# Kernel optimization log

Measured on AMD Instinct MI355X. Metric: run time of the kernel, lower is better.

Reference implementation:

```python
import jax, jax.numpy as jnp
import numpy as np

N = 100000
E = 1600000
D_IN = 128
D_OUT = 128


def setup_inputs() -> dict:
    key = jax.random.key(0)
    k1, k2, k3, k4, k5, k6 = jax.random.split(key, 6)
    h = jax.random.normal(k1, (N, D_IN), dtype=jnp.float32)
    # deg^{-1/2}-style positive per-node normalization, shape [N,1]
    norm = jax.random.uniform(k2, (N, 1), dtype=jnp.float32, minval=0.05, maxval=1.0)
    weight = jax.random.normal(k3, (D_IN, D_OUT), dtype=jnp.float32) * (1.0 / np.sqrt(D_IN))
    bias = jax.random.normal(k4, (D_OUT,), dtype=jnp.float32) * 0.01
    src = jax.random.randint(k5, (E,), 0, N, dtype=jnp.int32)
    dst = jax.random.randint(k6, (E,), 0, N, dtype=jnp.int32)
    return {"h": h, "norm": norm, "weight": weight, "bias": bias, "src": src, "dst": dst}


def reference(h, norm, weight, bias, src, dst):
    # m = (h @ W) * norm   (per-source-node message)
    m = jnp.matmul(h, weight) * norm            # [N, D_OUT]
    # copy_src + sum: scatter-sum messages from src nodes into dst nodes
    n = jax.ops.segment_sum(m[src], dst, num_segments=h.shape[0])  # [N, D_OUT]
    # destination-side normalization, bias, LeakyReLU(0.2)
    n = n * norm + bias
    return jax.nn.leaky_relu(n, negative_slope=0.2)
```

## Files before the change

kernel.cpp:

```cpp
#include <hip/hip_runtime.h>

#define N_NODES 100000
#define E_EDGES 1600000
#define D 128
#define SHIFT 7
#define BNODES 128
#define NB ((N_NODES + BNODES - 1) / BNODES)

#define CNT_CHUNK 2048
#define CNT_NBLK ((E_EDGES + CNT_CHUNK - 1) / CNT_CHUNK)
#define PREP_NBLK (N_NODES * 32 / 256)
#define PREP1K (N_NODES * 32 / 1024)
#define SCAT_CHUNK 8192
#define SCAT_PASS 2
#define SCAT_NBLK ((E_EDGES + SCAT_CHUNK - 1) / SCAT_CHUNK)
#define GATHD_NBLK ((N_NODES + 63) / 64)
#define GATH32_NBLK (N_NODES / 8)

#define CAPB 2560

#define CAP_N 64
#define LSTR 65

#define GROWS 64
#define KCH 32

typedef _Float16       f16x8  __attribute__((ext_vector_type(8)));
typedef float          f32x4  __attribute__((ext_vector_type(4)));
typedef unsigned short u16x8  __attribute__((ext_vector_type(8)));

#define WS_CNT   0
#define WS_POS   784
#define WS_BOFF  1568
#define WS_NOFF  2356
#define WS_EBUF  102400
#define WS_WHS   (WS_EBUF + NB * CAPB)
#define WS_ESRC  (102400 + E_EDGES)
#define WS_HS    (102400 + 2 * E_EDGES)
#define WS_FULL_INTS ((size_t)WS_HS + (size_t)N_NODES * D / 2)
#define WS_MID_INTS  ((size_t)WS_HS)

#define GROW16 256

__global__ __launch_bounds__(1024) void prep_scatter(
    const float* __restrict__ h, const float* __restrict__ norm,
    unsigned short* __restrict__ hs, const int* __restrict__ src,
    const int* __restrict__ dst, int* __restrict__ bcnt,
    int* __restrict__ ebuf, int prep_blocks)
{
    __shared__ int hist[NB];
    const int t = threadIdx.x;
    if ((int)blockIdx.x < prep_blocks) {
        const int idx = blockIdx.x * 1024 + t;
        const int node = idx >> 5;
        const int c = (idx & 31) << 2;
        const float nv = norm[node];
        const float4 v = *reinterpret_cast<const float4*>(h + node * D + c);
        float a[4] = {v.x * nv, v.y * nv, v.z * nv, v.w * nv};
        ushort4 o;
        unsigned short* op = reinterpret_cast<unsigned short*>(&o);
        #pragma unroll
        for (int i = 0; i < 4; ++i) {
            unsigned int u = __float_as_uint(a[i]);
            u += 0x7FFFu + ((u >> 16) & 1u);
            op[i] = (unsigned short)(u >> 16);
        }
        *reinterpret_cast<ushort4*>(hs + node * D + c) = o;
        return;
    }
    const int cb = blockIdx.x - prep_blocks;
    const int e0 = cb * SCAT_CHUNK;
    const int rem = (E_EDGES - e0 < SCAT_CHUNK) ? (E_EDGES - e0) : SCAT_CHUNK;
    for (int i = t; i < NB; i += 1024) hist[i] = 0;
    __syncthreads();

    if (rem == SCAT_CHUNK) {
        const int4* d4 = reinterpret_cast<const int4*>(dst + e0);
        #pragma unroll
        for (int p = 0; p < SCAT_PASS; ++p) {
            const int4 vv = d4[p * 1024 + t];
            atomicAdd(&hist[vv.x >> SHIFT], 1);
            atomicAdd(&hist[vv.y >> SHIFT], 1);
            atomicAdd(&hist[vv.z >> SHIFT], 1);
            atomicAdd(&hist[vv.w >> SHIFT], 1);
        }
    } else {
        for (int i = t; i < rem; i += 1024)
            atomicAdd(&hist[dst[e0 + i] >> SHIFT], 1);
    }
    __syncthreads();

    if (t < NB) {
        const int c = hist[t];
        hist[t] = c ? atomicAdd(&bcnt[t], c) : 0;
    }
    __syncthreads();

    if (rem == SCAT_CHUNK) {
        const int4* d4 = reinterpret_cast<const int4*>(dst + e0);
        const int4* s4 = reinterpret_cast<const int4*>(src + e0);
        #pragma unroll
        for (int p = 0; p < SCAT_PASS; ++p) {
            const int4 dv = d4[p * 1024 + t];
            const int4 sv = s4[p * 1024 + t];
            int b, pz;
            b = dv.x >> SHIFT; pz = atomicAdd(&hist[b], 1);
            if (pz < CAPB) ebuf[b * CAPB + pz] = (sv.x << SHIFT) | (dv.x & (BNODES - 1));
            b = dv.y >> SHIFT; pz = atomicAdd(&hist[b], 1);
            if (pz < CAPB) ebuf[b * CAPB + pz] = (sv.y << SHIFT) | (dv.y & (BNODES - 1));
            b = dv.z >> SHIFT; pz = atomicAdd(&hist[b], 1);
            if (pz < CAPB) ebuf[b * CAPB + pz] = (sv.z << SHIFT) | (dv.z & (BNODES - 1));
            b = dv.w >> SHIFT; pz = atomicAdd(&hist[b], 1);
            if (pz < CAPB) ebuf[b * CAPB + pz] = (sv.w << SHIFT) | (dv.w & (BNODES - 1));
        }
    } else {
        for (int i = t; i < rem; i += 1024) {
            const int d = dst[e0 + i];
            const int b = d >> SHIFT;
            const int pz = atomicAdd(&hist[b], 1);
            if (pz < CAPB) ebuf[b * CAPB + pz] = (src[e0 + i] << SHIFT) | (d & (BNODES - 1));
        }
    }
}

__device__ __forceinline__ void wprep_body(int tid, const float* __restrict__ Wm,
                                           f16x8* __restrict__ Whs) {
    const int kiter = tid >> 9;
    const int nt = (tid >> 6) & 7;
    const int lane = tid & 63;
    const int q = lane >> 4;
    const int col = nt * 16 + (lane & 15);
    f16x8 v;
    #pragma unroll
    for (int j = 0; j < 8; ++j)
        v[j] = (_Float16)Wm[(kiter * 32 + q * 8 + j) * D + col];
    Whs[tid] = v;
}

__global__ __launch_bounds__(256) void gather_direct(
    const unsigned short* __restrict__ hs, const int* __restrict__ bcnt,
    const int* __restrict__ ebuf, _Float16* __restrict__ g16,
    const float* __restrict__ Wm, f16x8* __restrict__ Whs)
{
    if ((int)blockIdx.x >= GATHD_NBLK) {
        wprep_body((blockIdx.x - GATHD_NBLK) * 256 + threadIdx.x, Wm, Whs);
        return;
    }
    __shared__ int lists[64][LSTR];
    __shared__ int lcnt[64];
    const int t = threadIdx.x;
    const int g = blockIdx.x;
    const int bin = g >> 1;
    const int sub = g & 1;
    if (t < 64) lcnt[t] = 0;
    __syncthreads();
    int cnt = bcnt[bin];
    cnt = (cnt < 0) ? 0 : ((cnt > CAPB) ? CAPB : cnt);
    const int b0 = bin * CAPB;
    const int b1 = b0 + cnt;
    for (int i = b0 + t; i < b1; i += 256) {
        const int w = ebuf[i];
        const int l = w & (BNODES - 1);
        const unsigned s = (unsigned)w >> SHIFT;
        if ((l >> 6) == sub && s < (unsigned)N_NODES) {
            const int p = atomicAdd(&lcnt[l & 63], 1);
            if (p < CAP_N) lists[l & 63][p] = (int)s;
        }
    }
    __syncthreads();

    const int grp = t >> 4;
    const int c = (t & 15) << 3;

    #pragma unroll 1
    for (int r = 0; r < 4; ++r) {
        const int local = r * 16 + grp;
        const int node = g * 64 + local;
        const int deg = lcnt[local];
        float a[8];
        #pragma unroll
        for (int j = 0; j < 8; ++j) a[j] = 0.f;

        if (deg <= CAP_N) {
            const int* lp = lists[local];
            int i = 0;
            for (; i + 7 < deg; i += 8) {
                const int s0 = lp[i];     const int s1 = lp[i + 1];
                const int s2 = lp[i + 2]; const int s3 = lp[i + 3];
                const int s4 = lp[i + 4]; const int s5 = lp[i + 5];
                const int s6 = lp[i + 6]; const int s7 = lp[i + 7];
                const u16x8 u0 = *reinterpret_cast<const u16x8*>(hs + s0 * D + c);
                const u16x8 u1 = *reinterpret_cast<const u16x8*>(hs + s1 * D + c);
                const u16x8 u2 = *reinterpret_cast<const u16x8*>(hs + s2 * D + c);
                const u16x8 u3 = *reinterpret_cast<const u16x8*>(hs + s3 * D + c);
                const u16x8 u4 = *reinterpret_cast<const u16x8*>(hs + s4 * D + c);
                const u16x8 u5 = *reinterpret_cast<const u16x8*>(hs + s5 * D + c);
                const u16x8 u6 = *reinterpret_cast<const u16x8*>(hs + s6 * D + c);
                const u16x8 u7 = *reinterpret_cast<const u16x8*>(hs + s7 * D + c);
                #pragma unroll
                for (int j = 0; j < 8; ++j) {
                    a[j] += __uint_as_float((unsigned int)u0[j] << 16);
                    a[j] += __uint_as_float((unsigned int)u1[j] << 16);
                    a[j] += __uint_as_float((unsigned int)u2[j] << 16);
                    a[j] += __uint_as_float((unsigned int)u3[j] << 16);
                    a[j] += __uint_as_float((unsigned int)u4[j] << 16);
                    a[j] += __uint_as_float((unsigned int)u5[j] << 16);
                    a[j] += __uint_as_float((unsigned int)u6[j] << 16);
                    a[j] += __uint_as_float((unsigned int)u7[j] << 16);
                }
            }
            if (i + 3 < deg) {
                const int s0 = lp[i];     const int s1 = lp[i + 1];
                const int s2 = lp[i + 2]; const int s3 = lp[i + 3];
                const u16x8 u0 = *reinterpret_cast<const u16x8*>(hs + s0 * D + c);
                const u16x8 u1 = *reinterpret_cast<const u16x8*>(hs + s1 * D + c);
                const u16x8 u2 = *reinterpret_cast<const u16x8*>(hs + s2 * D + c);
                const u16x8 u3 = *reinterpret_cast<const u16x8*>(hs + s3 * D + c);
                #pragma unroll
                for (int j = 0; j < 8; ++j) {
                    a[j] += __uint_as_float((unsigned int)u0[j] << 16);
                    a[j] += __uint_as_float((unsigned int)u1[j] << 16);
                    a[j] += __uint_as_float((unsigned int)u2[j] << 16);
                    a[j] += __uint_as_float((unsigned int)u3[j] << 16);
                }
                i += 4;
            }
            for (; i < deg; ++i) {
                const int s = lp[i];
                const u16x8 u = *reinterpret_cast<const u16x8*>(hs + s * D + c);
                #pragma unroll
                for (int j = 0; j < 8; ++j)
                    a[j] += __uint_as_float((unsigned int)u[j] << 16);
            }
        } else {
            const int myl = (sub << 6) | local;
            for (int i = b0; i < b1; ++i) {
                const int w = ebuf[i];
                const unsigned s = (unsigned)w >> SHIFT;
                if ((w & (BNODES - 1)) == myl && s < (unsigned)N_NODES) {
                    const u16x8 u = *reinterpret_cast<const u16x8*>(hs + s * D + c);
                    #pragma unroll
                    for (int j = 0; j < 8; ++j)
                        a[j] += __uint_as_float((unsigned int)u[j] << 16);
                }
            }
        }

        if (node < N_NODES) {
            f16x8 o;
            #pragma unroll
            for (int j = 0; j < 8; ++j) o[j] = (_Float16)a[j];
            *reinterpret_cast<f16x8*>(g16 + node * GROW16 + c) = o;
        }
    }
}

__global__ __launch_bounds__(256) void gemm_mfma_f16g(
    const _Float16* g16, float* out, const f16x8* __restrict__ Whs,
    const float* __restrict__ bias, const float* __restrict__ norm)
{
    __shared__ f16x8 Wlds[2048];
    const int t = threadIdx.x;
    const int row0 = blockIdx.x * 64;

    #pragma unroll
    for (int p = 0; p < 8; ++p)
        reinterpret_cast<float4*>(Wlds)[p * 256 + t] =
            reinterpret_cast<const float4*>(Whs)[p * 256 + t];
    __syncthreads();

    const int lane = t & 63;
    const int strip = t >> 6;
    const int q = lane >> 4;
    const int l15 = lane & 15;

    int mrow = row0 + strip * 16 + l15;
    if (mrow >= N_NODES) mrow = N_NODES - 1;

    f32x4 acc[8];
    #pragma unroll
    for (int i = 0; i < 8; ++i) acc[i] = (f32x4){0.f, 0.f, 0.f, 0.f};

    #pragma unroll
    for (int kiter = 0; kiter < 4; ++kiter) {
        const f16x8 a =
            *reinterpret_cast<const f16x8*>(g16 + mrow * GROW16 + kiter * 32 + q * 8);
        #pragma unroll
        for (int nt = 0; nt < 8; ++nt) {
            const f16x8 b = Wlds[(kiter * 8 + nt) * 64 + lane];
            acc[nt] = __builtin_amdgcn_mfma_f32_16x16x32_f16(a, b, acc[nt], 0, 0, 0);
        }
    }

    __syncthreads();

    float nrm[4];
    int mr[4];
    #pragma unroll
    for (int rgi = 0; rgi < 4; ++rgi) {
        mr[rgi] = row0 + strip * 16 + q * 4 + rgi;
        nrm[rgi] = (mr[rgi] < N_NODES) ? norm[mr[rgi]] : 0.f;
    }
    #pragma unroll
    for (int nt = 0; nt < 8; ++nt) {
        const int col = nt * 16 + l15;
        const float bc = bias[col];
        #pragma unroll
        for (int rgi = 0; rgi < 4; ++rgi) {
            if (mr[rgi] < N_NODES) {
                float v = acc[nt][rgi] * nrm[rgi] + bc;
                v = v > 0.f ? v : 0.2f * v;
                out[mr[rgi] * D + col] = v;
            }
        }
    }
}

__global__ __launch_bounds__(256) void prep_count(const float* __restrict__ h,
                                                  const float* __restrict__ norm,
                                                  unsigned short* __restrict__ hs,
                                                  const int* __restrict__ dst,
                                                  int* __restrict__ cnt,
                                                  int prep_blocks) {
    __shared__ int hist[NB];
    const int t = threadIdx.x;
    if ((int)blockIdx.x < prep_blocks) {
        const int idx = blockIdx.x * 256 + t;
        const int node = idx >> 5;
        const int c = (idx & 31) << 2;
        const float nv = norm[node];
        const float4 v = *reinterpret_cast<const float4*>(h + node * D + c);
        float a[4] = {v.x * nv, v.y * nv, v.z * nv, v.w * nv};
        ushort4 o;
        unsigned short* op = reinterpret_cast<unsigned short*>(&o);
        #pragma unroll
        for (int i = 0; i < 4; ++i) {
            unsigned int u = __float_as_uint(a[i]);
            u += 0x7FFFu + ((u >> 16) & 1u);
            op[i] = (unsigned short)(u >> 16);
        }
        *reinterpret_cast<ushort4*>(hs + node * D + c) = o;
        return;
    }
    const int cb = blockIdx.x - prep_blocks;
    const int e0 = cb * CNT_CHUNK;
    const int rem = (E_EDGES - e0 < CNT_CHUNK) ? (E_EDGES - e0) : CNT_CHUNK;
    for (int i = t; i < NB; i += 256) hist[i] = 0;
    __syncthreads();
    if (rem == CNT_CHUNK) {
        const int4* d4 = reinterpret_cast<const int4*>(dst + e0);
        #pragma unroll
        for (int p = 0; p < 2; ++p) {
            const int4 v = d4[p * 256 + t];
            atomicAdd(&hist[v.x >> SHIFT], 1);
            atomicAdd(&hist[v.y >> SHIFT], 1);
            atomicAdd(&hist[v.z >> SHIFT], 1);
            atomicAdd(&hist[v.w >> SHIFT], 1);
        }
    } else {
        for (int i = t; i < rem; i += 256)
            atomicAdd(&hist[dst[e0 + i] >> SHIFT], 1);
    }
    __syncthreads();
    for (int b = t; b < NB; b += 256) {
        const int c = hist[b];
        if (c) atomicAdd(&cnt[b], c);
    }
}

__global__ __launch_bounds__(1024) void coarse_scan(const int* __restrict__ cnt,
                                                    int* __restrict__ boff,
                                                    int* __restrict__ pos) {
    __shared__ int buf[2][1024];
    const int t = threadIdx.x;
    const int v = (t < NB) ? cnt[t] : 0;
    int pi = 0;
    buf[0][t] = v;
    __syncthreads();
    #pragma unroll
    for (int o = 1; o < 1024; o <<= 1) {
        const int nv = buf[pi][t] + (t >= o ? buf[pi][t - o] : 0);
        buf[1 - pi][t] = nv;
        pi = 1 - pi;
        __syncthreads();
    }
    if (t < NB) {
        const int excl = buf[pi][t] - v;
        boff[t] = excl;
        pos[t] = excl;
    }
    if (t == 0) boff[NB] = E_EDGES;
}

__global__ __launch_bounds__(1024) void coarse_scatter(const int* __restrict__ src,
                                                       const int* __restrict__ dst,
                                                       int* __restrict__ pos,
                                                       int* __restrict__ ebuf) {
    __shared__ int hist[NB];
    const int t = threadIdx.x;
    const int e0 = blockIdx.x * SCAT_CHUNK;
    const int rem = (E_EDGES - e0 < SCAT_CHUNK) ? (E_EDGES - e0) : SCAT_CHUNK;
    for (int i = t; i < NB; i += 1024) hist[i] = 0;
    __syncthreads();
    if (rem == SCAT_CHUNK) {
        const int4* d4 = reinterpret_cast<const int4*>(dst + e0);
        #pragma unroll
        for (int p = 0; p < SCAT_PASS; ++p) {
            const int4 v = d4[p * 1024 + t];
            atomicAdd(&hist[v.x >> SHIFT], 1);
            atomicAdd(&hist[v.y >> SHIFT], 1);
            atomicAdd(&hist[v.z >> SHIFT], 1);
            atomicAdd(&hist[v.w >> SHIFT], 1);
        }
    } else {
        for (int i = t; i < rem; i += 1024)
            atomicAdd(&hist[dst[e0 + i] >> SHIFT], 1);
    }
    __syncthreads();
    for (int b = t; b < NB; b += 1024) {
        const int c = hist[b];
        if (c) hist[b] = atomicAdd(&pos[b], c);
    }
    __syncthreads();
    if (rem == SCAT_CHUNK) {
        const int4* d4 = reinterpret_cast<const int4*>(dst + e0);
        const int4* s4 = reinterpret_cast<const int4*>(src + e0);
        #pragma unroll
        for (int p = 0; p < SCAT_PASS; ++p) {
            const int4 dv = d4[p * 1024 + t];
            const int4 sv = s4[p * 1024 + t];
            int pz;
            pz = atomicAdd(&hist[dv.x >> SHIFT], 1);
            ebuf[pz] = (sv.x << SHIFT) | (dv.x & (BNODES - 1));
            pz = atomicAdd(&hist[dv.y >> SHIFT], 1);
            ebuf[pz] = (sv.y << SHIFT) | (dv.y & (BNODES - 1));
            pz = atomicAdd(&hist[dv.z >> SHIFT], 1);
            ebuf[pz] = (sv.z << SHIFT) | (dv.z & (BNODES - 1));
            pz = atomicAdd(&hist[dv.w >> SHIFT], 1);
            ebuf[pz] = (sv.w << SHIFT) | (dv.w & (BNODES - 1));
        }
    } else {
        for (int i = t; i < rem; i += 1024) {
            const int d = dst[e0 + i];
            const int b = d >> SHIFT;
            const int p = atomicAdd(&hist[b], 1);
            ebuf[p] = (src[e0 + i] << SHIFT) | (d & (BNODES - 1));
        }
    }
}

__global__ __launch_bounds__(256) void bin_sort(const int* __restrict__ boff,
                                                const int* __restrict__ ebuf,
                                                int* __restrict__ esrc,
                                                int* __restrict__ noff) {
    __shared__ int hist[BNODES];
    __shared__ int curs[BNODES];
    __shared__ int sbuf[2][BNODES];
    const int t = threadIdx.x;
    const int bin = blockIdx.x;
    if (t < BNODES) hist[t] = 0;
    __syncthreads();
    const int b0 = boff[bin];
    const int b1 = boff[bin + 1];
    for (int i = b0 + t; i < b1; i += 256)
        atomicAdd(&hist[ebuf[i] & (BNODES - 1)], 1);
    __syncthreads();
    if (t < BNODES) sbuf[0][t] = hist[t];
    __syncthreads();
    int pi = 0;
    #pragma unroll
    for (int o = 1; o < BNODES; o <<= 1) {
        if (t < BNODES)
            sbuf[1 - pi][t] = sbuf[pi][t] + (t >= o ? sbuf[pi][t - o] : 0);
        pi = 1 - pi;
        __syncthreads();
    }
    if (t < BNODES) {
        const int base = b0 + sbuf[pi][t] - hist[t];
        curs[t] = base;
        const int node = (bin << SHIFT) + t;
        if (node < N_NODES) noff[node] = base;
    }
    if (bin == 0 && t == 0) noff[N_NODES] = E_EDGES;
    __syncthreads();
    for (int i = b0 + t; i < b1; i += 256) {
        const int w = ebuf[i];
        const int p = atomicAdd(&curs[w & (BNODES - 1)], 1);
        esrc[p] = w >> SHIFT;
    }
}

__global__ __launch_bounds__(256) void gather_fp32(const float* __restrict__ h,
                                                   const float* __restrict__ norm,
                                                   const int* __restrict__ noff,
                                                   const int* __restrict__ esrc,
                                                   float* __restrict__ g,
                                                   const float* __restrict__ Wm,
                                                   f16x8* __restrict__ Whs) {
    if ((int)blockIdx.x >= GATH32_NBLK) {
        wprep_body((blockIdx.x - GATH32_NBLK) * 256 + threadIdx.x, Wm, Whs);
        return;
    }
    const int t = threadIdx.x;
    const int node = blockIdx.x * 8 + (t >> 5);
    const int c = (t & 31) << 2;
    const int beg = noff[node];
    const int end = noff[node + 1];
    float4 acc = make_float4(0.f, 0.f, 0.f, 0.f);
    for (int i = beg; i < end; ++i) {
        const int s = esrc[i];
        const float nv = norm[s];
        const float4 hv = *reinterpret_cast<const float4*>(h + s * D + c);
        acc.x += hv.x * nv;
        acc.y += hv.y * nv;
        acc.z += hv.z * nv;
        acc.w += hv.w * nv;
    }
    *reinterpret_cast<float4*>(g + node * D + c) = acc;
}

__global__ __launch_bounds__(256) void scatter_kernel(
    const float* __restrict__ h, const float* __restrict__ norm,
    const int* __restrict__ src, const int* __restrict__ dst,
    float* __restrict__ g)
{
    const int idx = blockIdx.x * 256 + threadIdx.x;
    const int e = idx >> 5;
    const int c = (idx & 31) << 2;
    const int s = src[e];
    const int d = dst[e];
    const float nv = norm[s];
    const float4 hv = *reinterpret_cast<const float4*>(h + s * D + c);
    float* gp = g + d * D + c;
    atomicAdd(gp + 0, hv.x * nv);
    atomicAdd(gp + 1, hv.y * nv);
    atomicAdd(gp + 2, hv.z * nv);
    atomicAdd(gp + 3, hv.w * nv);
}

__global__ __launch_bounds__(256) void gemm_mfma(
    float* __restrict__ out, const f16x8* __restrict__ Whs,
    const float* __restrict__ bias, const float* __restrict__ norm)
{
    __shared__ f16x8 Wlds[2048];
    const int t = threadIdx.x;
    const int row0 = blockIdx.x * 64;

    #pragma unroll
    for (int p = 0; p < 8; ++p)
        reinterpret_cast<float4*>(Wlds)[p * 256 + t] =
            reinterpret_cast<const float4*>(Whs)[p * 256 + t];
    __syncthreads();

    const int lane = t & 63;
    const int strip = t >> 6;
    const int q = lane >> 4;
    const int l15 = lane & 15;

    int mrow = row0 + strip * 16 + l15;
    if (mrow >= N_NODES) mrow = N_NODES - 1;

    f32x4 acc[8];
    #pragma unroll
    for (int i = 0; i < 8; ++i) acc[i] = (f32x4){0.f, 0.f, 0.f, 0.f};

    #pragma unroll
    for (int kiter = 0; kiter < 4; ++kiter) {
        const float* gp = out + mrow * D + kiter * 32 + q * 8;
        const float4 ga = *reinterpret_cast<const float4*>(gp);
        const float4 gb = *reinterpret_cast<const float4*>(gp + 4);
        f16x8 a;
        a[0] = (_Float16)ga.x; a[1] = (_Float16)ga.y;
        a[2] = (_Float16)ga.z; a[3] = (_Float16)ga.w;
        a[4] = (_Float16)gb.x; a[5] = (_Float16)gb.y;
        a[6] = (_Float16)gb.z; a[7] = (_Float16)gb.w;
        #pragma unroll
        for (int nt = 0; nt < 8; ++nt) {
            const f16x8 b = Wlds[(kiter * 8 + nt) * 64 + lane];
            acc[nt] = __builtin_amdgcn_mfma_f32_16x16x32_f16(a, b, acc[nt], 0, 0, 0);
        }
    }

    float nrm[4];
    int mr[4];
    #pragma unroll
    for (int rgi = 0; rgi < 4; ++rgi) {
        mr[rgi] = row0 + strip * 16 + q * 4 + rgi;
        nrm[rgi] = (mr[rgi] < N_NODES) ? norm[mr[rgi]] : 0.f;
    }
    #pragma unroll
    for (int nt = 0; nt < 8; ++nt) {
        const int col = nt * 16 + l15;
        const float bc = bias[col];
        #pragma unroll
        for (int rgi = 0; rgi < 4; ++rgi) {
            if (mr[rgi] < N_NODES) {
                float v = acc[nt][rgi] * nrm[rgi] + bc;
                v = v > 0.f ? v : 0.2f * v;
                out[mr[rgi] * D + col] = v;
            }
        }
    }
}

__global__ __launch_bounds__(256) void gemm_epilogue(
    float* __restrict__ out, const float* __restrict__ Wm,
    const float* __restrict__ bias, const float* __restrict__ norm)
{
    __shared__ float gs[GROWS][D + 4];
    __shared__ float Wlds[KCH][D];
    const int t = threadIdx.x;
    const int row0 = blockIdx.x * GROWS;

    #pragma unroll
    for (int p = 0; p < 8; ++p) {
        const int i = p * 256 + t;
        const int r = i >> 5;
        const int c = (i & 31) << 2;
        int gr = row0 + r;
        if (gr >= N_NODES) gr = N_NODES - 1;
        const float4 v = *reinterpret_cast<const float4*>(out + gr * D + c);
        *reinterpret_cast<float4*>(&gs[r][c]) = v;
    }

    const int rg = (t >> 5) * 8;
    const int cb = (t & 31) << 2;

    float4 acc[8];
    #pragma unroll
    for (int i = 0; i < 8; ++i) acc[i] = make_float4(0.f, 0.f, 0.f, 0.f);

    for (int kc = 0; kc < D; kc += KCH) {
        __syncthreads();
        #pragma unroll
        for (int p = 0; p < 4; ++p) {
            const int i = p * 256 + t;
            const int kk = i >> 5;
            const int c = (i & 31) << 2;
            *reinterpret_cast<float4*>(&Wlds[kk][c]) =
                *reinterpret_cast<const float4*>(Wm + (kc + kk) * D + c);
        }
        __syncthreads();

        #pragma unroll
        for (int k4 = 0; k4 < KCH; k4 += 4) {
            float4 wv[4];
            #pragma unroll
            for (int kk = 0; kk < 4; ++kk)
                wv[kk] = *reinterpret_cast<const float4*>(&Wlds[k4 + kk][cb]);
            #pragma unroll
            for (int i = 0; i < 8; ++i) {
                const float4 gv = *reinterpret_cast<const float4*>(&gs[rg + i][kc + k4]);
                acc[i].x += gv.x * wv[0].x; acc[i].y += gv.x * wv[0].y;
                acc[i].z += gv.x * wv[0].z; acc[i].w += gv.x * wv[0].w;
                acc[i].x += gv.y * wv[1].x; acc[i].y += gv.y * wv[1].y;
                acc[i].z += gv.y * wv[1].z; acc[i].w += gv.y * wv[1].w;
                acc[i].x += gv.z * wv[2].x; acc[i].y += gv.z * wv[2].y;
                acc[i].z += gv.z * wv[2].z; acc[i].w += gv.z * wv[2].w;
                acc[i].x += gv.w * wv[3].x; acc[i].y += gv.w * wv[3].y;
                acc[i].z += gv.w * wv[3].z; acc[i].w += gv.w * wv[3].w;
            }
        }
    }

    const float4 b = *reinterpret_cast<const float4*>(bias + cb);
    #pragma unroll
    for (int i = 0; i < 8; ++i) {
        const int gr = row0 + rg + i;
        if (gr < N_NODES) {
            const float nv = norm[gr];
            float4 v;
            v.x = acc[i].x * nv + b.x;
            v.y = acc[i].y * nv + b.y;
            v.z = acc[i].z * nv + b.z;
            v.w = acc[i].w * nv + b.w;
            v.x = v.x > 0.f ? v.x : 0.2f * v.x;
            v.y = v.y > 0.f ? v.y : 0.2f * v.y;
            v.z = v.z > 0.f ? v.z : 0.2f * v.z;
            v.w = v.w > 0.f ? v.w : 0.2f * v.w;
            *reinterpret_cast<float4*>(out + gr * D + cb) = v;
        }
    }
}

extern "C" void kernel_launch(void* const* d_in, const int* in_sizes, int n_in,
                              void* d_out, int out_size, void* d_ws, size_t ws_size,
                              hipStream_t stream) {
    const float* h    = (const float*)d_in[0];
    const float* norm = (const float*)d_in[1];
    const float* Wm   = (const float*)d_in[2];
    const float* bias = (const float*)d_in[3];
    const int*   src  = (const int*)d_in[4];
    const int*   dst  = (const int*)d_in[5];
    float* out = (float*)d_out;
    int* ws = (int*)d_ws;

    if (ws_size >= WS_MID_INTS * 4) {
        const bool use_bf16 = (ws_size >= WS_FULL_INTS * 4);

        if (use_bf16) {
            int* bcnt = ws + WS_CNT;
            int* ebuf = ws + WS_EBUF;
            f16x8* Whs = (f16x8*)(ws + WS_WHS);
            unsigned short* hs = (unsigned short*)(ws + WS_HS);
            _Float16* g16 = (_Float16*)out;

            hipMemsetAsync(bcnt, 0, 784 * sizeof(int), stream);
            prep_scatter<<<PREP1K + SCAT_NBLK, 1024, 0, stream>>>(
                h, norm, hs, src, dst, bcnt, ebuf, PREP1K);
            gather_direct<<<GATHD_NBLK + 8, 256, 0, stream>>>(hs, bcnt, ebuf, g16, Wm, Whs);
            gemm_mfma_f16g<<<(N_NODES + 63) / 64, 256, 0, stream>>>(g16, out, Whs, bias, norm);
        } else {
            int* cnt  = ws + WS_CNT;
            int* pos  = ws + WS_POS;
            int* boff = ws + WS_BOFF;
            int* noff = ws + WS_NOFF;
            int* ebuf = ws + WS_EBUF;
            int* esrc = ws + WS_ESRC;
            f16x8* Whs = (f16x8*)ebuf;
            hipMemsetAsync(cnt, 0, 784 * sizeof(int), stream);
            prep_count<<<CNT_NBLK, 256, 0, stream>>>(h, norm, (unsigned short*)ws, dst, cnt, 0);
            coarse_scan   <<<1, 1024, 0, stream>>>(cnt, boff, pos);
            coarse_scatter<<<SCAT_NBLK, 1024, 0, stream>>>(src, dst, pos, ebuf);
            bin_sort      <<<NB, 256, 0, stream>>>(boff, ebuf, esrc, noff);
            gather_fp32<<<GATH32_NBLK + 8, 256, 0, stream>>>(h, norm, noff, esrc, out, Wm, Whs);
            gemm_mfma<<<(N_NODES + 63) / 64, 256, 0, stream>>>(out, Whs, bias, norm);
        }
    } else {
        hipMemsetAsync(out, 0, (size_t)N_NODES * D * sizeof(float), stream);
        scatter_kernel<<<(E_EDGES * 32) / 256, 256, 0, stream>>>(h, norm, src, dst, out);
        gemm_epilogue<<<(N_NODES + GROWS - 1) / GROWS, 256, 0, stream>>>(out, Wm, bias, norm);
    }
}
```

Baseline: 218.7 us.

## Fuse neighbor gather with MFMA GEMM epilogue in one kernel via LDS staging

Merges the gather kernel and the GEMM kernel. Each block writes its aggregated fp16 rows into shared memory, reusing the edge-list buffer with its stride widened, then runs the MFMA matmul directly from LDS. This removes the fp16 intermediate round trip through global memory and one kernel launch. In exchange, every block converts the weight matrix from fp32 to fp16 itself in two halves, and the added LDS use may lower occupancy.

```diff
diff --git a/kernel.cpp b/kernel.cpp
--- a/kernel.cpp
+++ b/kernel.cpp
@@ -20,7 +20,7 @@
 #define CAPB 2560
 
 #define CAP_N 64
-#define LSTR 65
+#define LSTR 68
 
 #define GROWS 64
 #define KCH 32
@@ -34,13 +34,10 @@
 #define WS_BOFF  1568
 #define WS_NOFF  2356
 #define WS_EBUF  102400
-#define WS_WHS   (WS_EBUF + NB * CAPB)
 #define WS_ESRC  (102400 + E_EDGES)
 #define WS_HS    (102400 + 2 * E_EDGES)
 #define WS_FULL_INTS ((size_t)WS_HS + (size_t)N_NODES * D / 2)
 #define WS_MID_INTS  ((size_t)WS_HS)
-
-#define GROW16 256
 
 __global__ __launch_bounds__(1024) void prep_scatter(
     const float* __restrict__ h, const float* __restrict__ norm,
@@ -123,31 +120,17 @@
     }
 }
 
-__device__ __forceinline__ void wprep_body(int tid, const float* __restrict__ Wm,
-                                           f16x8* __restrict__ Whs) {
-    const int kiter = tid >> 9;
-    const int nt = (tid >> 6) & 7;
-    const int lane = tid & 63;
-    const int q = lane >> 4;
-    const int col = nt * 16 + (lane & 15);
-    f16x8 v;
-    #pragma unroll
-    for (int j = 0; j < 8; ++j)
-        v[j] = (_Float16)Wm[(kiter * 32 + q * 8 + j) * D + col];
-    Whs[tid] = v;
-}
-
-__global__ __launch_bounds__(256) void gather_direct(
+__global__ __launch_bounds__(256) void gather_gemm(
     const unsigned short* __restrict__ hs, const int* __restrict__ bcnt,
-    const int* __restrict__ ebuf, _Float16* __restrict__ g16,
-    const float* __restrict__ Wm, f16x8* __restrict__ Whs)
+    const int* __restrict__ ebuf, const float* __restrict__ Wm,
+    const float* __restrict__ bias, const float* __restrict__ norm,
+    float* __restrict__ out)
 {
-    if ((int)blockIdx.x >= GATHD_NBLK) {
-        wprep_body((blockIdx.x - GATHD_NBLK) * 256 + threadIdx.x, Wm, Whs);
-        return;
-    }
     __shared__ int lists[64][LSTR];
     __shared__ int lcnt[64];
+    __shared__ f16x8 Wlds[1024];
+    _Float16 (*gs)[136] = reinterpret_cast<_Float16 (*)[136]>(&lists[0][0]);
+
     const int t = threadIdx.x;
     const int g = blockIdx.x;
     const int bin = g >> 1;
@@ -175,7 +158,6 @@
     #pragma unroll 1
     for (int r = 0; r < 4; ++r) {
         const int local = r * 16 + grp;
-        const int node = g * 64 + local;
         const int deg = lcnt[local];
         float a[8];
         #pragma unroll
@@ -246,53 +228,51 @@
             }
         }
 
-        if (node < N_NODES) {
-            f16x8 o;
-            #pragma unroll
-            for (int j = 0; j < 8; ++j) o[j] = (_Float16)a[j];
-            *reinterpret_cast<f16x8*>(g16 + node * GROW16 + c) = o;
-        }
-    }
-}
-
-__global__ __launch_bounds__(256) void gemm_mfma_f16g(
-    const _Float16* g16, float* out, const f16x8* __restrict__ Whs,
-    const float* __restrict__ bias, const float* __restrict__ norm)
-{
-    __shared__ f16x8 Wlds[2048];
-    const int t = threadIdx.x;
-    const int row0 = blockIdx.x * 64;
-
-    #pragma unroll
-    for (int p = 0; p < 8; ++p)
-        reinterpret_cast<float4*>(Wlds)[p * 256 + t] =
-            reinterpret_cast<const float4*>(Whs)[p * 256 + t];
-    __syncthreads();
+        f16x8 o;
+        #pragma unroll
+        for (int j = 0; j < 8; ++j) o[j] = (_Float16)a[j];
+        *reinterpret_cast<f16x8*>(&gs[local][c]) = o;
+    }
 
     const int lane = t & 63;
     const int strip = t >> 6;
     const int q = lane >> 4;
     const int l15 = lane & 15;
-
-    int mrow = row0 + strip * 16 + l15;
-    if (mrow >= N_NODES) mrow = N_NODES - 1;
+    const int row0 = g * 64;
 
     f32x4 acc[8];
     #pragma unroll
     for (int i = 0; i < 8; ++i) acc[i] = (f32x4){0.f, 0.f, 0.f, 0.f};
 
-    #pragma unroll
-    for (int kiter = 0; kiter < 4; ++kiter) {
-        const f16x8 a =
-            *reinterpret_cast<const f16x8*>(g16 + mrow * GROW16 + kiter * 32 + q * 8);
-        #pragma unroll
-        for (int nt = 0; nt < 8; ++nt) {
-            const f16x8 b = Wlds[(kiter * 8 + nt) * 64 + lane];
-            acc[nt] = __builtin_amdgcn_mfma_f32_16x16x32_f16(a, b, acc[nt], 0, 0, 0);
-        }
-    }
-
-    __syncthreads();
+    #pragma unroll 1
+    for (int half = 0; half < 2; ++half) {
+        __syncthreads();
+        for (int e = t; e < 1024; e += 256) {
+            const int ge = (half << 10) + e;
+            const int kiter = ge >> 9;
+            const int nt = (ge >> 6) & 7;
+            const int lane2 = ge & 63;
+            const int q2 = lane2 >> 4;
+            const int col = nt * 16 + (lane2 & 15);
+            f16x8 v;
+            #pragma unroll
+            for (int j = 0; j < 8; ++j)
+                v[j] = (_Float16)Wm[(kiter * 32 + q2 * 8 + j) * D + col];
+            Wlds[e] = v;
+        }
+        __syncthreads();
+        #pragma unroll
+        for (int kk = 0; kk < 2; ++kk) {
+            const int kiter = half * 2 + kk;
+            const f16x8 a =
+                *reinterpret_cast<const f16x8*>(&gs[strip * 16 + l15][kiter * 32 + q * 8]);
+            #pragma unroll
+            for (int nt = 0; nt < 8; ++nt) {
+                const f16x8 b = Wlds[(kk * 8 + nt) * 64 + lane];
+                acc[nt] = __builtin_amdgcn_mfma_f32_16x16x32_f16(a, b, acc[nt], 0, 0, 0);
+            }
+        }
+    }
 
     float nrm[4];
     int mr[4];
@@ -488,6 +468,20 @@
         const int p = atomicAdd(&curs[w & (BNODES - 1)], 1);
         esrc[p] = w >> SHIFT;
     }
+}
+
+__device__ __forceinline__ void wprep_body(int tid, const float* __restrict__ Wm,
+                                           f16x8* __restrict__ Whs) {
+    const int kiter = tid >> 9;
+    const int nt = (tid >> 6) & 7;
+    const int lane = tid & 63;
+    const int q = lane >> 4;
+    const int col = nt * 16 + (lane & 15);
+    f16x8 v;
+    #pragma unroll
+    for (int j = 0; j < 8; ++j)
+        v[j] = (_Float16)Wm[(kiter * 32 + q * 8 + j) * D + col];
+    Whs[tid] = v;
 }
 
 __global__ __launch_bounds__(256) void gather_fp32(const float* __restrict__ h,
@@ -701,15 +695,12 @@
         if (use_bf16) {
             int* bcnt = ws + WS_CNT;
             int* ebuf = ws + WS_EBUF;
-            f16x8* Whs = (f16x8*)(ws + WS_WHS);
             unsigned short* hs = (unsigned short*)(ws + WS_HS);
-            _Float16* g16 = (_Float16*)out;
 
             hipMemsetAsync(bcnt, 0, 784 * sizeof(int), stream);
             prep_scatter<<<PREP1K + SCAT_NBLK, 1024, 0, stream>>>(
                 h, norm, hs, src, dst, bcnt, ebuf, PREP1K);
-            gather_direct<<<GATHD_NBLK + 8, 256, 0, stream>>>(hs, bcnt, ebuf, g16, Wm, Whs);
-            gemm_mfma_f16g<<<(N_NODES + 63) / 64, 256, 0, stream>>>(g16, out, Whs, bias, norm);
+            gather_gemm<<<GATHD_NBLK, 256, 0, stream>>>(hs, bcnt, ebuf, Wm, bias, norm, out);
         } else {
             int* cnt  = ws + WS_CNT;
             int* pos  = ws + WS_POS;
```

Result: faster. 212.5 us (-2.8%).
